# Kernel optimization log

Measured on AMD Instinct MI355X. Metric: run time of the kernel, lower is better.

## Reference

```python
import jax, jax.numpy as jnp
import numpy as np

N_NODES = 65536
N_EDGES = 1048576
IN_F = 128
HID_F = 128
OUT_F = 128


def setup_inputs() -> dict:
    key = jax.random.key(0)
    ks = jax.random.split(key, 8)
    feat = jax.random.normal(ks[0], (N_NODES, IN_F), dtype=jnp.float32)
    eweight = jax.random.uniform(ks[1], (N_EDGES, 1), dtype=jnp.float32)
    W1 = jax.random.normal(ks[2], (IN_F, HID_F), dtype=jnp.float32) * (1.0 / np.sqrt(IN_F))
    b1 = jnp.zeros((HID_F,), dtype=jnp.float32)
    W2 = jax.random.normal(ks[3], (HID_F, OUT_F), dtype=jnp.float32) * (1.0 / np.sqrt(HID_F))
    b2 = jnp.zeros((OUT_F,), dtype=jnp.float32)
    src = jax.random.randint(ks[4], (N_EDGES,), 0, N_NODES, dtype=jnp.int32)
    dst = jax.random.randint(ks[5], (N_EDGES,), 0, N_NODES, dtype=jnp.int32)
    return {"feat": feat, "eweight": eweight, "W1": W1, "b1": b1,
            "W2": W2, "b2": b2, "src": src, "dst": dst}


def _degrees(src, dst, n_nodes):
    ones = jnp.ones(src.shape[0], dtype=jnp.float32)
    deg_out = jax.ops.segment_sum(ones, src, num_segments=n_nodes)
    deg_in = jax.ops.segment_sum(ones, dst, num_segments=n_nodes)
    # DGL GraphConv clamps degree to min 1 before norm='both'
    return jnp.clip(deg_out, 1.0, None), jnp.clip(deg_in, 1.0, None)


def _graph_conv(feat, W, b, src, dst, out_norm, in_norm, n_nodes):
    # DGL GraphConv, norm='both': D_out^{-1/2} x -> x W -> spmm sum -> D_in^{-1/2} -> + b
    h = feat * out_norm[:, None]
    h = h @ W
    agg = jax.ops.segment_sum(h[src], dst, num_segments=n_nodes)
    return agg * in_norm[:, None] + b


def reference(feat, eweight, W1, b1, W2, b2, src, dst):
    n = feat.shape[0]
    deg_out, deg_in = _degrees(src, dst, n)
    out_norm = jax.lax.rsqrt(deg_out)
    in_norm = jax.lax.rsqrt(deg_in)
    h = _graph_conv(feat, W1, b1, src, dst, out_norm, in_norm, n)
    h = jax.nn.relu(h)
    h = _graph_conv(h, W2, b2, src, dst, out_norm, in_norm, n)
    # final update_all: u_mul_e + sum (eweight given)
    msg = h[src] * eweight  # [E, OUT_F]
    return jax.ops.segment_sum(msg, dst, num_segments=n)
```

## Files before the change

### kernel.cpp

```cpp
#include <hip/hip_runtime.h>

#define F 128
#define NN 65536
#define NBA 512
#define NBS 128
#define COARSE 256
#define CAP_BIN 4864
#define CAP_CSR 5632

typedef unsigned int uint;
typedef unsigned short ushort;
typedef unsigned char uchar;
typedef __attribute__((ext_vector_type(8))) short short8;
typedef __attribute__((ext_vector_type(8))) unsigned short ushort8;
typedef __attribute__((ext_vector_type(4))) float floatx4;
typedef __attribute__((ext_vector_type(4))) uint uintx4;

__device__ __forceinline__ ushort f2bf(float f) {
  uint u = __float_as_uint(f);
  u += 0x7fffu + ((u >> 16) & 1u);
  return (ushort)(u >> 16);
}


__global__ __launch_bounds__(256) void w_prep(const float* __restrict__ W1,
                                              const float* __restrict__ W2,
                                              ushort* __restrict__ W1t,
                                              ushort* __restrict__ W2t,
                                              int* __restrict__ cursorD,
                                              int* __restrict__ cursorS) {
  int b = blockIdx.x;
  if (b == 0) cursorD[threadIdx.x] = 0;
  if (b == 1) cursorS[threadIdx.x] = 0;
  const float* W = (b < 64) ? W1 : W2;
  ushort* Wt = (b < 64) ? W1t : W2t;
  int idx = (b & 63) * 256 + threadIdx.x;
  int k = idx >> 7, n = idx & 127;
  Wt[n * F + k] = f2bf(W[idx]);
}

__global__ __launch_bounds__(256) void bin_edges(
    const int* __restrict__ src, const int* __restrict__ dst,
    const float* __restrict__ ew, int E,
    int* __restrict__ cursorD, int* __restrict__ cursorS,
    uint2* __restrict__ slotD, uchar* __restrict__ srcF) {
  __shared__ int cnt[4][COARSE];
  __shared__ int base[COARSE];
  bool isD = blockIdx.x < NBA;
  int blk = isD ? blockIdx.x : blockIdx.x - NBA;
  int nblk = isD ? NBA : NBS;
  const int* key = isD ? dst : src;
  int* cursor = isD ? cursorD : cursorS;
  int wave = threadIdx.x >> 6;
  for (int i = threadIdx.x; i < 4 * COARSE; i += 256) ((int*)cnt)[i] = 0;
  __syncthreads();
  int chunk = (E + nblk - 1) / nblk;
  int s0 = blk * chunk, s1 = min(E, s0 + chunk);
  for (int i = s0 + threadIdx.x; i < s1; i += 256)
    atomicAdd(&cnt[wave][key[i] >> 8], 1);
  __syncthreads();
  if (threadIdx.x < COARSE) {
    int b = threadIdx.x;
    int tot = cnt[0][b] + cnt[1][b] + cnt[2][b] + cnt[3][b];
    base[b] = tot ? atomicAdd(&cursor[b], tot) : 0;
    cnt[0][b] = 0;
  }
  __syncthreads();
  if (isD) {
    for (int i = s0 + threadIdx.x; i < s1; i += 256) {
      int d = dst[i];
      int bin = d >> 8;
      int p = base[bin] + atomicAdd(&cnt[0][bin], 1);
      if (p < CAP_BIN) {
        uint2 v;
        v.x = (uint)(src[i] & 0xffff) | ((uint)f2bf(ew[i]) << 16);
        v.y = (uint)(d & 255);
        slotD[(size_t)bin * CAP_BIN + p] = v;
      }
    }
  } else {
    for (int i = s0 + threadIdx.x; i < s1; i += 256) {
      int s = src[i];
      int bin = s >> 8;
      int p = base[bin] + atomicAdd(&cnt[0][bin], 1);
      if (p < CAP_BIN) srcF[(size_t)bin * CAP_BIN + p] = (uchar)(s & 255);
    }
  }
}

__global__ __launch_bounds__(1024) void bucket_csr(
    const uint2* __restrict__ slotD, const int* __restrict__ cursorD,
    int2* __restrict__ rowRange, float* __restrict__ inNorm, uint* __restrict__ csr,
    const uchar* __restrict__ srcF, const int* __restrict__ cursorS,
    float* __restrict__ outNorm) {
  __shared__ int hist[256], base[256], cur[256];
  int t = threadIdx.x;
  if (blockIdx.x >= COARSE) {
    int b = blockIdx.x - COARSE;
    int lo = b * CAP_BIN;
    int cntS = min(cursorS[b], CAP_BIN);
    if (t < 256) hist[t] = 0;
    __syncthreads();
    for (int i = lo + t; i < lo + cntS; i += 1024)
      atomicAdd(&hist[srcF[i]], 1);
    __syncthreads();
    if (t < 256) outNorm[b * 256 + t] = rsqrtf((float)max(hist[t], 1));
    return;
  }
  int b = blockIdx.x;
  int lo = b * CAP_BIN;
  int cntD = min(cursorD[b], CAP_BIN);
  int hi = lo + cntD;
  if (t < 256) hist[t] = 0;
  __syncthreads();
  for (int i = lo + t; i < hi; i += 1024)
    atomicAdd(&hist[slotD[i].y], 1);
  __syncthreads();
  if (t < 256) base[t] = (hist[t] + 3) & ~3;
  __syncthreads();
  for (int off = 1; off < 256; off <<= 1) {
    int x = 0;
    if (t < 256 && t >= off) x = base[t - off];
    __syncthreads();
    if (t < 256) base[t] += x;
    __syncthreads();
  }
  if (t < 256) {
    int v = hist[t];
    int sz4 = (v + 3) & ~3;
    int st = b * CAP_CSR + base[t] - sz4;
    base[t] = st;
    cur[t] = 0;
    int node = b * 256 + t;
    rowRange[node] = make_int2(st, v);
    inNorm[node] = rsqrtf((float)max(v, 1));
    for (int p = st + v; p < st + sz4; ++p) csr[p] = 0x80000000u;
  }
  __syncthreads();
  for (int i = lo + t; i < hi; i += 1024) {
    uint2 v = slotD[i];
    int fine = v.y;
    int p = base[fine] + atomicAdd(&cur[fine], 1);
    csr[p] = v.x;
  }
}

template <bool BF16IN>
__global__ __launch_bounds__(256) void gemm_mfma(
    const void* __restrict__ Xv, const float* __restrict__ scale,
    const ushort* __restrict__ Wt, ushort* __restrict__ Y) {
  __shared__ ushort sA[128 * 136];
  __shared__ ushort sB[128 * 136];
  int t = threadIdx.x;
  int row0 = blockIdx.x * 128;

  {
    int r = t >> 1, hf = t & 1;
    ushort* ap = sA + r * 136 + hf * 64;
    if (BF16IN) {
      const ushort* xp = (const ushort*)Xv;
#pragma unroll
      for (int j = 0; j < 8; ++j) {
        int q = 2 * hf + (j >> 2);
        *(ushort8*)(ap + j * 8) =
            *(const ushort8*)(xp + ((size_t)q * NN + row0 + r) * 32 + (j & 3) * 8);
      }
    } else {
      const float* xp = (const float*)Xv + (size_t)(row0 + r) * F + hf * 64;
      float s = scale[row0 + r];
#pragma unroll
      for (int j = 0; j < 8; ++j) {
        float4 v0 = *(const float4*)(xp + j * 8);
        float4 v1 = *(const float4*)(xp + j * 8 + 4);
        ushort8 o;
        o[0] = f2bf(v0.x * s); o[1] = f2bf(v0.y * s); o[2] = f2bf(v0.z * s); o[3] = f2bf(v0.w * s);
        o[4] = f2bf(v1.x * s); o[5] = f2bf(v1.y * s); o[6] = f2bf(v1.z * s); o[7] = f2bf(v1.w * s);
        *(ushort8*)(ap + j * 8) = o;
      }
    }
  }
  {
    int n = t >> 1, hf = t & 1;
    const ushort* wp = Wt + n * F + hf * 64;
    ushort* bp = sB + n * 136 + hf * 64;
#pragma unroll
    for (int j = 0; j < 8; ++j)
      *(ushort8*)(bp + j * 8) = *(const ushort8*)(wp + j * 8);
  }
  __syncthreads();

  int lane = t & 63, wave = t >> 6;
  int quad = lane >> 4, l16 = lane & 15;
  int mrow0 = wave * 32;

  floatx4 acc[2][8];
#pragma unroll
  for (int a = 0; a < 2; ++a)
#pragma unroll
    for (int c = 0; c < 8; ++c) acc[a][c] = (floatx4){0.f, 0.f, 0.f, 0.f};

#pragma unroll
  for (int kc = 0; kc < 128; kc += 32) {
    short8 afrag[2], bfrag[8];
#pragma unroll
    for (int a = 0; a < 2; ++a)
      afrag[a] = *(const short8*)(sA + (mrow0 + a * 16 + l16) * 136 + kc + quad * 8);
#pragma unroll
    for (int c = 0; c < 8; ++c)
      bfrag[c] = *(const short8*)(sB + (c * 16 + l16) * 136 + kc + quad * 8);
#pragma unroll
    for (int a = 0; a < 2; ++a)
#pragma unroll
      for (int c = 0; c < 8; ++c)
        acc[a][c] = __builtin_amdgcn_mfma_f32_16x16x32_bf16(afrag[a], bfrag[c], acc[a][c], 0, 0, 0);
  }

#pragma unroll
  for (int a = 0; a < 2; ++a)
#pragma unroll
    for (int c = 0; c < 8; ++c)
#pragma unroll
      for (int r = 0; r < 4; ++r) {
        int row = row0 + mrow0 + a * 16 + quad * 4 + r;
        int col = c * 16 + l16;
        Y[((size_t)(col >> 5) * NN + row) * 32 + (col & 31)] = f2bf(acc[a][c][r]);
      }
}


template <bool EW, bool NB, bool RELU, bool PS, bool OUT_BF16>
__global__ __launch_bounds__(256) void spmm(
    const ushort* __restrict__ hb, const int2* __restrict__ rowRange,
    const uint* __restrict__ csr, const float* __restrict__ inNorm,
    const float* __restrict__ bias, const float* __restrict__ postScale,
    void* __restrict__ outv) {
  int bid = blockIdx.x;
  int plane = bid >> 10;
  int chunkId = bid & 1023;
  int lane = threadIdx.x & 63;
  int g = lane >> 2;
  int j = lane & 3;
  int n = chunkId * 64 + (threadIdx.x >> 6) * 16 + g;
  int2 r = rowRange[n];
  int len4 = (r.y + 3) & ~3;
  const char* pb = (const char*)hb + (size_t)plane * ((size_t)NN * 64);
  uint joff = (uint)j << 4;
  float acc[8] = {0.f, 0.f, 0.f, 0.f, 0.f, 0.f, 0.f, 0.f};

#define GQ(e, c, q_)                                                     \
  {                                                                      \
    uint ei = (e);                                                       \
    c = *(const uint4*)(pb + (((ei & 0xffffu) << 6) | joff));            \
    q_ = EW ? __uint_as_float(ei & 0xffff0000u)                          \
            : ((int)ei >= 0 ? 1.0f : 0.0f);                              \
  }
#define ACC8(c, q_)                                                     \
  {                                                                     \
    acc[0] = fmaf(__uint_as_float(c.x << 16), q_, acc[0]);              \
    acc[1] = fmaf(__uint_as_float(c.x & 0xffff0000u), q_, acc[1]);      \
    acc[2] = fmaf(__uint_as_float(c.y << 16), q_, acc[2]);              \
    acc[3] = fmaf(__uint_as_float(c.y & 0xffff0000u), q_, acc[3]);      \
    acc[4] = fmaf(__uint_as_float(c.z << 16), q_, acc[4]);              \
    acc[5] = fmaf(__uint_as_float(c.z & 0xffff0000u), q_, acc[5]);      \
    acc[6] = fmaf(__uint_as_float(c.w << 16), q_, acc[6]);              \
    acc[7] = fmaf(__uint_as_float(c.w & 0xffff0000u), q_, acc[7]);      \
  }

  int i = 0;
  while (i + 8 <= len4) {
    uintx4 e0 = __builtin_nontemporal_load((const uintx4*)(csr + r.x + i));
    uintx4 e1 = __builtin_nontemporal_load((const uintx4*)(csr + r.x + i + 4));
    uint4 c0, c1, c2, c3, c4, c5, c6, c7;
    float q0, q1, q2, q3, q4, q5, q6, q7;
    GQ(e0.x, c0, q0) GQ(e0.y, c1, q1) GQ(e0.z, c2, q2) GQ(e0.w, c3, q3)
    GQ(e1.x, c4, q4) GQ(e1.y, c5, q5) GQ(e1.z, c6, q6) GQ(e1.w, c7, q7)
    ACC8(c0, q0) ACC8(c1, q1) ACC8(c2, q2) ACC8(c3, q3)
    ACC8(c4, q4) ACC8(c5, q5) ACC8(c6, q6) ACC8(c7, q7)
    i += 8;
  }
  if (i < len4) {
    uintx4 e0 = __builtin_nontemporal_load((const uintx4*)(csr + r.x + i));
    uint4 c0, c1, c2, c3;
    float q0, q1, q2, q3;
    GQ(e0.x, c0, q0) GQ(e0.y, c1, q1) GQ(e0.z, c2, q2) GQ(e0.w, c3, q3)
    ACC8(c0, q0) ACC8(c1, q1) ACC8(c2, q2) ACC8(c3, q3)
  }
#undef GQ
#undef ACC8

  if (NB) {
    float sc = inNorm[n];
    float4 b0 = ((const float4*)bias)[plane * 8 + j * 2];
    float4 b1 = ((const float4*)bias)[plane * 8 + j * 2 + 1];
    float bb[8] = {b0.x, b0.y, b0.z, b0.w, b1.x, b1.y, b1.z, b1.w};
#pragma unroll
    for (int k = 0; k < 8; ++k) {
      acc[k] = fmaf(acc[k], sc, bb[k]);
      if (RELU) acc[k] = fmaxf(acc[k], 0.f);
    }
    if (PS) {
      float o = postScale[n];
#pragma unroll
      for (int k = 0; k < 8; ++k) acc[k] *= o;
    }
  }
  if (OUT_BF16) {
    uintx4 o;
    o.x = ((uint)f2bf(acc[1]) << 16) | (uint)f2bf(acc[0]);
    o.y = ((uint)f2bf(acc[3]) << 16) | (uint)f2bf(acc[2]);
    o.z = ((uint)f2bf(acc[5]) << 16) | (uint)f2bf(acc[4]);
    o.w = ((uint)f2bf(acc[7]) << 16) | (uint)f2bf(acc[6]);
    __builtin_nontemporal_store(o, (uintx4*)outv + ((size_t)plane * NN + n) * 4 + j);
  } else {
    floatx4 lo = {acc[0], acc[1], acc[2], acc[3]};
    floatx4 hi = {acc[4], acc[5], acc[6], acc[7]};
    __builtin_nontemporal_store(lo, (floatx4*)outv + (size_t)n * 32 + plane * 8 + j * 2);
    __builtin_nontemporal_store(hi, (floatx4*)outv + (size_t)n * 32 + plane * 8 + j * 2 + 1);
  }
}


extern "C" void kernel_launch(void* const* d_in, const int* in_sizes, int n_in,
                              void* d_out, int out_size, void* d_ws, size_t ws_size,
                              hipStream_t stream) {
  const float* feat = (const float*)d_in[0];
  const float* ew   = (const float*)d_in[1];
  const float* W1   = (const float*)d_in[2];
  const float* b1   = (const float*)d_in[3];
  const float* W2   = (const float*)d_in[4];
  const float* b2   = (const float*)d_in[5];
  const int*   src  = (const int*)d_in[6];
  const int*   dst  = (const int*)d_in[7];
  const int N = in_sizes[0] / F;
  const int E = in_sizes[6];
  float* out = (float*)d_out;

  char* ws = (char*)d_ws;
  size_t off = 0;
  auto alloc = [&](size_t bytes) {
    void* p = ws + off;
    off += (bytes + 255) & ~(size_t)255;
    return p;
  };
  int2*   rowRange = (int2*)alloc((size_t)N * 8);
  float*  inNorm   = (float*)alloc((size_t)N * 4);
  float*  outNorm  = (float*)alloc((size_t)N * 4);
  ushort* W1t      = (ushort*)alloc((size_t)F * F * 2);
  ushort* W2t      = (ushort*)alloc((size_t)F * F * 2);
  int*    cursorD  = (int*)alloc(COARSE * 4);
  int*    cursorS  = (int*)alloc(COARSE * 4);
  uint*   csr      = (uint*)alloc((size_t)COARSE * CAP_CSR * 4);
  ushort* bufAb    = (ushort*)alloc((size_t)N * F * 2);
  ushort* bufBb    = (ushort*)alloc((size_t)N * F * 2);
  ushort* bufCb    = (ushort*)alloc((size_t)N * F * 2);
  if (off > ws_size) return;

  uint2* slotD;
  uchar* srcF;
  {
    char* tp = (char*)bufBb;
    size_t toff = 0;
    auto talloc = [&](size_t bytes) {
      void* p = tp + toff;
      toff += (bytes + 255) & ~(size_t)255;
      return p;
    };
    slotD = (uint2*)talloc((size_t)COARSE * CAP_BIN * 8);
    srcF  = (uchar*)talloc((size_t)COARSE * CAP_BIN);
  }

  w_prep<<<128, 256, 0, stream>>>(W1, W2, W1t, W2t, cursorD, cursorS);
  bin_edges<<<NBA + NBS, 256, 0, stream>>>(src, dst, ew, E, cursorD, cursorS, slotD, srcF);
  bucket_csr<<<2 * COARSE, 1024, 0, stream>>>(slotD, cursorD, rowRange, inNorm, csr,
                                              srcF, cursorS, outNorm);

  gemm_mfma<false><<<N / 128, 256, 0, stream>>>(feat, outNorm, W1t, bufAb);
  spmm<false, true, true, true, true><<<N / 16, 256, 0, stream>>>(
      bufAb, rowRange, csr, inNorm, b1, outNorm, bufBb);
  gemm_mfma<true><<<N / 128, 256, 0, stream>>>(bufBb, nullptr, W2t, bufAb);
  spmm<false, true, false, false, true><<<N / 16, 256, 0, stream>>>(
      bufAb, rowRange, csr, inNorm, b2, nullptr, bufCb);
  spmm<true, false, false, false, false><<<N / 16, 256, 0, stream>>>(
      bufCb, rowRange, csr, nullptr, nullptr, nullptr, out);
}
```

Baseline: 307.2 us.

## Interleave spmm blocks across planes, prefetch CSR indices, drop nontemporal hints

```diff
diff --git a/kernel.cpp b/kernel.cpp
--- a/kernel.cpp
+++ b/kernel.cpp
@@ -14,7 +14,6 @@
 typedef __attribute__((ext_vector_type(8))) short short8;
 typedef __attribute__((ext_vector_type(8))) unsigned short ushort8;
 typedef __attribute__((ext_vector_type(4))) float floatx4;
-typedef __attribute__((ext_vector_type(4))) uint uintx4;
 
 __device__ __forceinline__ ushort f2bf(float f) {
   uint u = __float_as_uint(f);
@@ -235,12 +234,12 @@
     const float* __restrict__ bias, const float* __restrict__ postScale,
     void* __restrict__ outv) {
   int bid = blockIdx.x;
-  int plane = bid >> 10;
-  int chunkId = bid & 1023;
+  int plane = (bid & 7) >> 1;
+  int chunk = ((bid >> 3) << 1) | (bid & 1);
   int lane = threadIdx.x & 63;
   int g = lane >> 2;
   int j = lane & 3;
-  int n = chunkId * 64 + (threadIdx.x >> 6) * 16 + g;
+  int n = chunk * 64 + (threadIdx.x >> 6) * 16 + g;
   int2 r = rowRange[n];
   int len4 = (r.y + 3) & ~3;
   const char* pb = (const char*)hb + (size_t)plane * ((size_t)NN * 64);
@@ -267,22 +266,32 @@
   }
 
   int i = 0;
+  uint4 e0, e1;
+  if (i + 8 <= len4) {
+    e0 = *(const uint4*)(csr + r.x);
+    e1 = *(const uint4*)(csr + r.x + 4);
+  }
   while (i + 8 <= len4) {
-    uintx4 e0 = __builtin_nontemporal_load((const uintx4*)(csr + r.x + i));
-    uintx4 e1 = __builtin_nontemporal_load((const uintx4*)(csr + r.x + i + 4));
     uint4 c0, c1, c2, c3, c4, c5, c6, c7;
     float q0, q1, q2, q3, q4, q5, q6, q7;
     GQ(e0.x, c0, q0) GQ(e0.y, c1, q1) GQ(e0.z, c2, q2) GQ(e0.w, c3, q3)
     GQ(e1.x, c4, q4) GQ(e1.y, c5, q5) GQ(e1.z, c6, q6) GQ(e1.w, c7, q7)
+    uint4 f0, f1;
+    bool more = (i + 16 <= len4);
+    if (more) {
+      f0 = *(const uint4*)(csr + r.x + i + 8);
+      f1 = *(const uint4*)(csr + r.x + i + 12);
+    }
     ACC8(c0, q0) ACC8(c1, q1) ACC8(c2, q2) ACC8(c3, q3)
     ACC8(c4, q4) ACC8(c5, q5) ACC8(c6, q6) ACC8(c7, q7)
+    if (more) { e0 = f0; e1 = f1; }
     i += 8;
   }
   if (i < len4) {
-    uintx4 e0 = __builtin_nontemporal_load((const uintx4*)(csr + r.x + i));
+    uint4 t0 = *(const uint4*)(csr + r.x + i);
     uint4 c0, c1, c2, c3;
     float q0, q1, q2, q3;
-    GQ(e0.x, c0, q0) GQ(e0.y, c1, q1) GQ(e0.z, c2, q2) GQ(e0.w, c3, q3)
+    GQ(t0.x, c0, q0) GQ(t0.y, c1, q1) GQ(t0.z, c2, q2) GQ(t0.w, c3, q3)
     ACC8(c0, q0) ACC8(c1, q1) ACC8(c2, q2) ACC8(c3, q3)
   }
 #undef GQ
@@ -305,17 +314,17 @@
     }
   }
   if (OUT_BF16) {
-    uintx4 o;
+    uint4 o;
     o.x = ((uint)f2bf(acc[1]) << 16) | (uint)f2bf(acc[0]);
     o.y = ((uint)f2bf(acc[3]) << 16) | (uint)f2bf(acc[2]);
     o.z = ((uint)f2bf(acc[5]) << 16) | (uint)f2bf(acc[4]);
     o.w = ((uint)f2bf(acc[7]) << 16) | (uint)f2bf(acc[6]);
-    __builtin_nontemporal_store(o, (uintx4*)outv + ((size_t)plane * NN + n) * 4 + j);
+    ((uint4*)outv)[((size_t)plane * NN + n) * 4 + j] = o;
   } else {
-    floatx4 lo = {acc[0], acc[1], acc[2], acc[3]};
-    floatx4 hi = {acc[4], acc[5], acc[6], acc[7]};
-    __builtin_nontemporal_store(lo, (floatx4*)outv + (size_t)n * 32 + plane * 8 + j * 2);
-    __builtin_nontemporal_store(hi, (floatx4*)outv + (size_t)n * 32 + plane * 8 + j * 2 + 1);
+    float4 lo = {acc[0], acc[1], acc[2], acc[3]};
+    float4 hi = {acc[4], acc[5], acc[6], acc[7]};
+    ((float4*)outv)[(size_t)n * 32 + plane * 8 + j * 2] = lo;
+    ((float4*)outv)[(size_t)n * 32 + plane * 8 + j * 2 + 1] = hi;
   }
 }
 
```

After: 259.1 us, median of 2. 15.7% less time.
